# Performance work log

Measured on AMD Instinct MI355X. Metric: run time of the kernel, lower is better.

## Reference

```python
import jax, jax.numpy as jnp
import numpy as np
from jax import lax

VOCAB, EMBED, HIDDEN, LAYERS = 32000, 512, 1024, 2
B, S = 16, 256


def _lstm_layer(x_seq, h0, c0, W_ih, W_hh, b_ih, b_hh):
    # x_seq: [B, S, D]; PyTorch gate order: i, f, g, o
    def step(carry, x_t):
        h, c = carry
        gates = x_t @ W_ih.T + b_ih + h @ W_hh.T + b_hh  # [B, 4H]
        i, f, g, o = jnp.split(gates, 4, axis=-1)
        i = jax.nn.sigmoid(i); f = jax.nn.sigmoid(f)
        g = jnp.tanh(g); o = jax.nn.sigmoid(o)
        c = f * c + i * g
        h = o * jnp.tanh(c)
        return (h, c), h
    (hT, cT), hs = lax.scan(step, (h0, c0), jnp.swapaxes(x_seq, 0, 1))
    return jnp.swapaxes(hs, 0, 1), hT, cT  # [B,S,H], [B,H], [B,H]


def setup_inputs() -> dict:
    key = jax.random.key(0)
    ks = jax.random.split(key, 8)
    s_e = 1.0 / np.sqrt(EMBED)
    s_h = 1.0 / np.sqrt(HIDDEN)
    return {
        "x": jax.random.randint(ks[0], (B, S), 0, VOCAB),
        "h0": jnp.zeros((LAYERS, B, HIDDEN), jnp.float32),
        "c0": jnp.zeros((LAYERS, B, HIDDEN), jnp.float32),
        "emb": jax.random.normal(ks[1], (VOCAB, EMBED), jnp.float32),
        "W_ih0": jax.random.normal(ks[2], (4 * HIDDEN, EMBED), jnp.float32) * s_e,
        "W_hh0": jax.random.normal(ks[3], (4 * HIDDEN, HIDDEN), jnp.float32) * s_h,
        "b_ih0": jnp.zeros((4 * HIDDEN,), jnp.float32),
        "b_hh0": jnp.zeros((4 * HIDDEN,), jnp.float32),
        "W_ih1": jax.random.normal(ks[4], (4 * HIDDEN, HIDDEN), jnp.float32) * s_h,
        "W_hh1": jax.random.normal(ks[5], (4 * HIDDEN, HIDDEN), jnp.float32) * s_h,
        "b_ih1": jnp.zeros((4 * HIDDEN,), jnp.float32),
        "b_hh1": jnp.zeros((4 * HIDDEN,), jnp.float32),
        "fc_W": jax.random.normal(ks[6], (VOCAB, HIDDEN), jnp.float32) * s_h,
        "fc_b": jnp.zeros((VOCAB,), jnp.float32),
    }


def reference(x, h0, c0, emb, W_ih0, W_hh0, b_ih0, b_hh0,
              W_ih1, W_hh1, b_ih1, b_hh1, fc_W, fc_b):
    h = emb[x]  # [B, S, E] embedding lookup
    h, h1, c1 = _lstm_layer(h, h0[0], c0[0], W_ih0, W_hh0, b_ih0, b_hh0)
    h, h2, c2 = _lstm_layer(h, h0[1], c0[1], W_ih1, W_hh1, b_ih1, b_hh1)
    logits = h @ fc_W.T + fc_b  # [B, S, V]
    hT = jnp.stack([h1, h2])    # [L, B, H]
    cT = jnp.stack([c1, c2])
    return logits, hT, cT
```

## Files before the change

### kernel.cpp

```cpp
#include <hip/hip_runtime.h>
#include <hip/hip_bf16.h>
#include <cmath>

#define BATCH 16
#define SEQ 256
#define EMBED 512
#define HIDDEN 1024
#define GATES 4096
#define VOCAB 32000
#define MROWS 4096
#define LOGITS_SZ 131072000

#define NSLOT 257
#define SEQ_SLOTU16 16384
#define SEQ_LOU16 (NSLOT * SEQ_SLOTU16)

typedef unsigned int u32;
typedef unsigned short u16;
typedef unsigned long long u64;
typedef __attribute__((ext_vector_type(8))) short bf16x8;
typedef __attribute__((ext_vector_type(4))) float f32x4;

#define AS1 __attribute__((address_space(1)))
#define AS3 __attribute__((address_space(3)))

__device__ __forceinline__ u32 f2bf(float f) {
    u32 u = __float_as_uint(f);
    return (u + 0x7fffu + ((u >> 16) & 1u)) >> 16;
}
__device__ __forceinline__ float bf2f(u32 b) { return __uint_as_float(b << 16); }

__device__ __forceinline__ void astore(u64* p, u64 v) {
    __hip_atomic_store(p, v, __ATOMIC_RELAXED, __HIP_MEMORY_SCOPE_AGENT);
}

__global__ void embed_kernel(const int* __restrict__ x, const float* __restrict__ emb,
                             float* __restrict__ X0) {
    int r = blockIdx.x;
    int s = r >> 4, b = r & 15;
    int tok = x[b * SEQ + s];
    const float4* src = (const float4*)(emb + (size_t)tok * EMBED);
    float4* dst = (float4*)(X0 + (size_t)r * EMBED);
    for (int i = threadIdx.x; i < EMBED / 4; i += blockDim.x) dst[i] = src[i];
}

__global__ __launch_bounds__(256) void gemm_bt(
    const float* __restrict__ A, const float* __restrict__ B,
    const float* __restrict__ b1, const float* __restrict__ b2,
    float* __restrict__ C, int M, int N, int K, int perm) {
    __shared__ float As[8][128];
    __shared__ float Bs[8][128];
    int tid = threadIdx.x;
    int bm = blockIdx.y, bn = blockIdx.x;
    int arow = tid >> 1;
    int ak4 = (tid & 1) * 4;
    const float* Ag = A + (size_t)(bm * 128 + arow) * K + ak4;
    const float* Bg = B + (size_t)(bn * 128 + arow) * K + ak4;
    int tx = tid & 15, ty = tid >> 4;

    float acc[8][8];
#pragma unroll
    for (int i = 0; i < 8; i++)
#pragma unroll
        for (int j = 0; j < 8; j++) acc[i][j] = 0.f;

    for (int k0 = 0; k0 < K; k0 += 8) {
        float4 a4 = *(const float4*)(Ag + k0);
        float4 b4 = *(const float4*)(Bg + k0);
        __syncthreads();
        As[ak4 + 0][arow] = a4.x; As[ak4 + 1][arow] = a4.y;
        As[ak4 + 2][arow] = a4.z; As[ak4 + 3][arow] = a4.w;
        Bs[ak4 + 0][arow] = b4.x; Bs[ak4 + 1][arow] = b4.y;
        Bs[ak4 + 2][arow] = b4.z; Bs[ak4 + 3][arow] = b4.w;
        __syncthreads();
#pragma unroll
        for (int k = 0; k < 8; k++) {
            float av[8], bv[8];
            *(float4*)(av + 0) = *(const float4*)&As[k][ty * 8 + 0];
            *(float4*)(av + 4) = *(const float4*)&As[k][ty * 8 + 4];
            *(float4*)(bv + 0) = *(const float4*)&Bs[k][tx * 8 + 0];
            *(float4*)(bv + 4) = *(const float4*)&Bs[k][tx * 8 + 4];
#pragma unroll
            for (int i = 0; i < 8; i++)
#pragma unroll
                for (int j = 0; j < 8; j++) acc[i][j] += av[i] * bv[j];
        }
    }

#pragma unroll
    for (int i = 0; i < 8; i++) {
        int r = bm * 128 + ty * 8 + i;
        int orow = perm ? ((r & 15) * SEQ + (r >> 4)) : r;
#pragma unroll
        for (int j = 0; j < 8; j += 4) {
            int c = bn * 128 + tx * 8 + j;
            float4 v;
            float bb0 = (b1 ? b1[c + 0] : 0.f) + (b2 ? b2[c + 0] : 0.f);
            float bb1 = (b1 ? b1[c + 1] : 0.f) + (b2 ? b2[c + 1] : 0.f);
            float bb2 = (b1 ? b1[c + 2] : 0.f) + (b2 ? b2[c + 2] : 0.f);
            float bb3 = (b1 ? b1[c + 3] : 0.f) + (b2 ? b2[c + 3] : 0.f);
            v.x = acc[i][j + 0] + bb0;
            v.y = acc[i][j + 1] + bb1;
            v.z = acc[i][j + 2] + bb2;
            v.w = acc[i][j + 3] + bb3;
            *(float4*)&C[(size_t)orow * N + c] = v;
        }
    }
}

__global__ __launch_bounds__(256) void f32_to_bf16_kernel(
    const float* __restrict__ in, u16* __restrict__ out, int n8) {
    for (int i = blockIdx.x * 256 + threadIdx.x; i < n8; i += gridDim.x * 256) {
        float4 a = ((const float4*)in)[2 * (size_t)i + 0];
        float4 b = ((const float4*)in)[2 * (size_t)i + 1];
        uint4 o;
        o.x = f2bf(a.x) | (f2bf(a.y) << 16);
        o.y = f2bf(a.z) | (f2bf(a.w) << 16);
        o.z = f2bf(b.x) | (f2bf(b.y) << 16);
        o.w = f2bf(b.z) | (f2bf(b.w) << 16);
        ((uint4*)out)[i] = o;
    }
}

__global__ __launch_bounds__(256) void wih_swizzle_kernel(
    const float* __restrict__ W, u16* __restrict__ hi, u16* __restrict__ lo) {
    int bid = blockIdx.x, tid = threadIdx.x;
    int j0 = bid * 4;
#pragma unroll
    for (int i = 0; i < 8; i++) {
        int q = i * 256 + tid;
        int s32 = q >> 6, l = q & 63;
        int row = l & 15, hi4 = l >> 4;
        int nrow = (row >> 2) * HIDDEN + j0 + (row & 3);
        int k = s32 * 32 + hi4 * 8;
        const float* src = W + (size_t)nrow * HIDDEN + k;
        u32 hw[4], lw[4];
#pragma unroll
        for (int e = 0; e < 4; e++) {
            float x0 = src[2 * e], x1 = src[2 * e + 1];
            u32 h0 = f2bf(x0), h1 = f2bf(x1);
            hw[e] = h0 | (h1 << 16);
            lw[e] = f2bf(x0 - bf2f(h0)) | (f2bf(x1 - bf2f(h1)) << 16);
        }
        size_t e0 = (size_t)bid * 2048 + q;
        ((uint4*)hi)[e0] = make_uint4(hw[0], hw[1], hw[2], hw[3]);
        ((uint4*)lo)[e0] = make_uint4(lw[0], lw[1], lw[2], lw[3]);
    }
}

__global__ __launch_bounds__(256) void fc_mfma(
    const u16* __restrict__ Abf,
    const u16* __restrict__ Bbf,
    const float* __restrict__ bias,
    float* __restrict__ C) {
    const int K = HIDDEN;
    const int N = VOCAB;
    __shared__ char smem[16384];
    char* As = smem;
    char* Bs = smem + 8192;

    int tid = threadIdx.x;
    int w = tid >> 6, l = tid & 63;
    int bn = blockIdx.x, bm = blockIdx.y;
    int wr = w >> 1, wc = w & 1;
    int lr = l & 15, lk = l >> 4;

    f32x4 acc[4][4];
#pragma unroll
    for (int m = 0; m < 4; m++)
#pragma unroll
        for (int n = 0; n < 4; n++) acc[m][n] = {0.f, 0.f, 0.f, 0.f};

    int srow = tid >> 2, skc = (tid & 3) * 8;
    const u16* ga0 = Abf + (size_t)(bm * 128 + srow) * K + skc;
    const u16* ga1 = Abf + (size_t)(bm * 128 + 64 + srow) * K + skc;
    const u16* gb0 = Bbf + (size_t)(bn * 128 + srow) * K + skc;
    const u16* gb1 = Bbf + (size_t)(bn * 128 + 64 + srow) * K + skc;
    char* la0 = As + w * 1024;
    char* la1 = As + 4096 + w * 1024;
    char* lb0 = Bs + w * 1024;
    char* lb1 = Bs + 4096 + w * 1024;

    int afo[4], bfo[4];
#pragma unroll
    for (int m = 0; m < 4; m++) afo[m] = (wr * 64 + m * 16 + lr) * 64 + lk * 16;
#pragma unroll
    for (int n = 0; n < 4; n++) bfo[n] = (wc * 64 + n * 16 + lr) * 64 + lk * 16;

    for (int k0 = 0; k0 < K; k0 += 32) {
        __syncthreads();
        __builtin_amdgcn_global_load_lds((const AS1 u32*)(const void*)(ga0 + k0),
                                         (AS3 u32*)(void*)la0, 16, 0, 0);
        __builtin_amdgcn_global_load_lds((const AS1 u32*)(const void*)(ga1 + k0),
                                         (AS3 u32*)(void*)la1, 16, 0, 0);
        __builtin_amdgcn_global_load_lds((const AS1 u32*)(const void*)(gb0 + k0),
                                         (AS3 u32*)(void*)lb0, 16, 0, 0);
        __builtin_amdgcn_global_load_lds((const AS1 u32*)(const void*)(gb1 + k0),
                                         (AS3 u32*)(void*)lb1, 16, 0, 0);
        __syncthreads();

        bf16x8 af[4], bfr[4];
#pragma unroll
        for (int m = 0; m < 4; m++) af[m] = *(const bf16x8*)(As + afo[m]);
#pragma unroll
        for (int n = 0; n < 4; n++) bfr[n] = *(const bf16x8*)(Bs + bfo[n]);
#pragma unroll
        for (int m = 0; m < 4; m++)
#pragma unroll
            for (int n = 0; n < 4; n++)
                acc[m][n] = __builtin_amdgcn_mfma_f32_16x16x32_bf16(
                    af[m], bfr[n], acc[m][n], 0, 0, 0);
    }

    int rbase = bm * 128 + wr * 64 + lk * 4;
    int cbase = bn * 128 + wc * 64 + lr;
#pragma unroll
    for (int m = 0; m < 4; m++) {
#pragma unroll
        for (int n = 0; n < 4; n++) {
            int c = cbase + n * 16;
            float bb = bias[c];
#pragma unroll
            for (int j = 0; j < 4; j++) {
                int r = rbase + m * 16 + j;
                int orow = (r & 15) * SEQ + (r >> 4);
                C[(size_t)orow * N + c] = acc[m][n][j] + bb;
            }
        }
    }
}

__global__ __launch_bounds__(256, 1) void lstm_fused(
    const float* __restrict__ Whh0, const float* __restrict__ Whh1,
    const float* __restrict__ G0,
    const u16* __restrict__ wih_hi,
    const u16* __restrict__ wih_lo,
    const float* __restrict__ bi1, const float* __restrict__ bh1,
    const float* __restrict__ c0in,
    float* __restrict__ c_tail, float* __restrict__ h_tail,
    u16* __restrict__ seq0, u16* __restrict__ seq1,
    u32* __restrict__ arrive) {
    __shared__ __align__(16) char lds[139264];
    char* W0hi = lds;
    char* W0lo = lds + 32768;
    char* W1hi = lds + 65536;
    char* W1lo = lds + 98304;
    float* Pw = (float*)(lds + 131072);

    const int tid = threadIdx.x;
    const int bid = blockIdx.x;
    const int j0 = bid * 4;
    const int w = tid >> 6, l = tid & 63;
    const int lb = l & 15, hi4 = l >> 4, xr = l & 7;

#pragma unroll
    for (int lay = 0; lay < 2; lay++) {
        const float* Whh = lay ? Whh1 : Whh0;
        char* dH = lay ? W1hi : W0hi;
        char* dL = lay ? W1lo : W0lo;
        for (int i = 0; i < 8; i++) {
            int q = i * 256 + tid;
            int row = q >> 7, cin = q & 127;
            int nrow = (row >> 2) * HIDDEN + j0 + (row & 3);
            const float* src = Whh + (size_t)nrow * HIDDEN + cin * 8;
            int dst = row * 2048 + ((cin ^ (row & 7)) << 4);
            u32 hw[4], lw[4];
#pragma unroll
            for (int e = 0; e < 4; e++) {
                float x0 = src[2 * e], x1 = src[2 * e + 1];
                u32 hb0 = f2bf(x0), hb1 = f2bf(x1);
                hw[e] = hb0 | (hb1 << 16);
                lw[e] = f2bf(x0 - bf2f(hb0)) | (f2bf(x1 - bf2f(hb1)) << 16);
            }
            *(uint4*)(dH + dst) = make_uint4(hw[0], hw[1], hw[2], hw[3]);
            *(uint4*)(dL + dst) = make_uint4(lw[0], lw[1], lw[2], lw[3]);
        }
    }

    float c0r = 0.f, c1r = 0.f;
    float g00 = 0, g01 = 0, g02 = 0, g03 = 0;
    float g10 = 0, g11 = 0, g12 = 0, g13 = 0;
    if (tid < 64) {
        c0r = c0in[lb * HIDDEN + j0 + hi4];
        c1r = c0in[16384 + lb * HIDDEN + j0 + hi4];
        const float* gp = G0 + (size_t)lb * GATES + j0 + hi4;
        g00 = gp[0]; g01 = gp[HIDDEN]; g02 = gp[2 * HIDDEN]; g03 = gp[3 * HIDDEN];
        g10 = bi1[j0 + hi4] + bh1[j0 + hi4];
        g11 = bi1[HIDDEN + j0 + hi4] + bh1[HIDDEN + j0 + hi4];
        g12 = bi1[2 * HIDDEN + j0 + hi4] + bh1[2 * HIDDEN + j0 + hi4];
        g13 = bi1[3 * HIDDEN + j0 + hi4] + bh1[3 * HIDDEN + j0 + hi4];
    }
    __syncthreads();

    const u64* s0h = (const u64*)seq0;
    const u64* s0l = (const u64*)(seq0 + SEQ_LOU16);
    const u64* s1h = (const u64*)seq1;
    const u64* s1l = (const u64*)(seq1 + SEQ_LOU16);
    const int fb = lb * 256 + hi4 * 2;
    const size_t wbase = (size_t)bid * 2048 + l;

    union u4bf { uint4 u; bf16x8 v; };

    for (int s = 0; s <= SEQ; s++) {
        const bool actL0 = (s < SEQ);
        const bool actL1 = (s >= 1);

        u4bf xh8[8], xl8[8], yh8[8], yl8[8];
        {
            const int base = s * 4096 + fb;
#pragma unroll
            for (int ss = 0; ss < 8; ss++) {
                const int idx = base + (w * 8 + ss) * 8;
                xh8[ss].u = *(const uint4*)(s0h + idx);
                xl8[ss].u = *(const uint4*)(s0l + idx);
            }
        }
        if (actL1) {
            const int base = (s - 1) * 4096 + fb;
#pragma unroll
            for (int ss = 0; ss < 8; ss++) {
                const int idx = base + (w * 8 + ss) * 8;
                yh8[ss].u = *(const uint4*)(s1h + idx);
                yl8[ss].u = *(const uint4*)(s1l + idx);
            }
        }

        if (actL0) {
            f32x4 a0 = {0.f,0.f,0.f,0.f}, a1 = {0.f,0.f,0.f,0.f}, a2 = {0.f,0.f,0.f,0.f};
#pragma unroll
            for (int ss = 0; ss < 8; ss++) {
                const int s32 = w * 8 + ss;
                const int off = lb * 2048 + (((s32 * 4 + hi4) ^ xr) << 4);
                bf16x8 ah = *(const bf16x8*)(W0hi + off);
                bf16x8 al = *(const bf16x8*)(W0lo + off);
                a0 = __builtin_amdgcn_mfma_f32_16x16x32_bf16(ah, xh8[ss].v, a0, 0, 0, 0);
                a1 = __builtin_amdgcn_mfma_f32_16x16x32_bf16(al, xh8[ss].v, a1, 0, 0, 0);
                a2 = __builtin_amdgcn_mfma_f32_16x16x32_bf16(ah, xl8[ss].v, a2, 0, 0, 0);
            }
            f32x4 v0 = a0 + a1 + a2;
            *(f32x4*)&Pw[((0 * 4 + w) * 64 + l) * 4] = v0;
        }

        if (actL1) {
            f32x4 a0 = {0.f,0.f,0.f,0.f}, a1 = {0.f,0.f,0.f,0.f}, a2 = {0.f,0.f,0.f,0.f};
#pragma unroll
            for (int ss = 0; ss < 8; ss++) {
                const size_t e = wbase + (size_t)(w * 8 + ss) * 64;
                bf16x8 ah = *(const bf16x8*)(wih_hi + e * 8);
                bf16x8 al = *(const bf16x8*)(wih_lo + e * 8);
                a0 = __builtin_amdgcn_mfma_f32_16x16x32_bf16(ah, xh8[ss].v, a0, 0, 0, 0);
                a1 = __builtin_amdgcn_mfma_f32_16x16x32_bf16(al, xh8[ss].v, a1, 0, 0, 0);
                a2 = __builtin_amdgcn_mfma_f32_16x16x32_bf16(ah, xl8[ss].v, a2, 0, 0, 0);
            }
#pragma unroll
            for (int ss = 0; ss < 8; ss++) {
                const int s32 = w * 8 + ss;
                const int off = lb * 2048 + (((s32 * 4 + hi4) ^ xr) << 4);
                bf16x8 ah = *(const bf16x8*)(W1hi + off);
                bf16x8 al = *(const bf16x8*)(W1lo + off);
                a0 = __builtin_amdgcn_mfma_f32_16x16x32_bf16(ah, yh8[ss].v, a0, 0, 0, 0);
                a1 = __builtin_amdgcn_mfma_f32_16x16x32_bf16(al, yh8[ss].v, a1, 0, 0, 0);
                a2 = __builtin_amdgcn_mfma_f32_16x16x32_bf16(ah, yl8[ss].v, a2, 0, 0, 0);
            }
            f32x4 v1 = a0 + a1 + a2;
            *(f32x4*)&Pw[((1 * 4 + w) * 64 + l) * 4] = v1;
        }
        __syncthreads();

        if (tid < 64) {
            if (actL0) {
                float pre[4];
#pragma unroll
                for (int g = 0; g < 4; g++) {
                    const int ll = (g << 4) | lb;
                    pre[g] = Pw[((0 * 4 + 0) * 64 + ll) * 4 + hi4]
                           + Pw[((0 * 4 + 1) * 64 + ll) * 4 + hi4]
                           + Pw[((0 * 4 + 2) * 64 + ll) * 4 + hi4]
                           + Pw[((0 * 4 + 3) * 64 + ll) * 4 + hi4];
                }
                const float ig = 1.f / (1.f + __expf(-(pre[0] + g00)));
                const float fg = 1.f / (1.f + __expf(-(pre[1] + g01)));
                const float gt = tanhf(pre[2] + g02);
                const float og = 1.f / (1.f + __expf(-(pre[3] + g03)));
                c0r = fg * c0r + ig * gt;
                const float hv = og * tanhf(c0r);
                if (s == SEQ - 1) {
                    h_tail[lb * HIDDEN + j0 + hi4] = hv;
                    c_tail[lb * HIDDEN + j0 + hi4] = c0r;
                }
                float q0 = __shfl(hv, 0 + l), q1 = __shfl(hv, 16 + l);
                float q2 = __shfl(hv, 32 + l), q3 = __shfl(hv, 48 + l);
                if (l < 16) {
                    u32 hb0 = f2bf(q0), hb1 = f2bf(q1), hb2 = f2bf(q2), hb3 = f2bf(q3);
                    u64 hq = (u64)(hb0 | (hb1 << 16)) | ((u64)(hb2 | (hb3 << 16)) << 32);
                    u32 lb0 = f2bf(q0 - bf2f(hb0)), lb1 = f2bf(q1 - bf2f(hb1));
                    u32 lb2 = f2bf(q2 - bf2f(hb2)), lb3 = f2bf(q3 - bf2f(hb3));
                    u64 lq = (u64)(lb0 | (lb1 << 16)) | ((u64)(lb2 | (lb3 << 16)) << 32);
                    const int iq = (s + 1) * 4096 + l * 256 + bid;
                    astore((u64*)seq0 + iq, hq);
                    astore((u64*)(seq0 + SEQ_LOU16) + iq, lq);
                }
            }
            if (actL1) {
                float pre[4];
#pragma unroll
                for (int g = 0; g < 4; g++) {
                    const int ll = (g << 4) | lb;
                    pre[g] = Pw[((1 * 4 + 0) * 64 + ll) * 4 + hi4]
                           + Pw[((1 * 4 + 1) * 64 + ll) * 4 + hi4]
                           + Pw[((1 * 4 + 2) * 64 + ll) * 4 + hi4]
                           + Pw[((1 * 4 + 3) * 64 + ll) * 4 + hi4];
                }
                const float ig = 1.f / (1.f + __expf(-(pre[0] + g10)));
                const float fg = 1.f / (1.f + __expf(-(pre[1] + g11)));
                const float gt = tanhf(pre[2] + g12);
                const float og = 1.f / (1.f + __expf(-(pre[3] + g13)));
                c1r = fg * c1r + ig * gt;
                const float hv = og * tanhf(c1r);
                if (s == SEQ) {
                    h_tail[16384 + lb * HIDDEN + j0 + hi4] = hv;
                    c_tail[16384 + lb * HIDDEN + j0 + hi4] = c1r;
                }
                float q0 = __shfl(hv, 0 + l), q1 = __shfl(hv, 16 + l);
                float q2 = __shfl(hv, 32 + l), q3 = __shfl(hv, 48 + l);
                if (l < 16) {
                    u32 hb0 = f2bf(q0), hb1 = f2bf(q1), hb2 = f2bf(q2), hb3 = f2bf(q3);
                    u64 hq = (u64)(hb0 | (hb1 << 16)) | ((u64)(hb2 | (hb3 << 16)) << 32);
                    u32 lb0 = f2bf(q0 - bf2f(hb0)), lb1 = f2bf(q1 - bf2f(hb1));
                    u32 lb2 = f2bf(q2 - bf2f(hb2)), lb3 = f2bf(q3 - bf2f(hb3));
                    u64 lq = (u64)(lb0 | (lb1 << 16)) | ((u64)(lb2 | (lb3 << 16)) << 32);
                    const int iq = s * 4096 + l * 256 + bid;
                    astore((u64*)seq1 + iq, hq);
                    astore((u64*)(seq1 + SEQ_LOU16) + iq, lq);
                }
            }
        }

        if (s < SEQ) {
            if (tid < 64) {
                asm volatile("s_waitcnt vmcnt(0)" ::: "memory");
                if (tid == 0)
                    __hip_atomic_store(&arrive[bid], (u32)(s + 1), __ATOMIC_RELAXED,
                                       __HIP_MEMORY_SCOPE_AGENT);
                if (s + 1 < SEQ) {
                    const float* gp = G0 + (size_t)((s + 1) * BATCH + lb) * GATES + j0 + hi4;
                    g00 = gp[0]; g01 = gp[HIDDEN];
                    g02 = gp[2 * HIDDEN]; g03 = gp[3 * HIDDEN];
                }
                const u32 epoch = (u32)(s + 1);
                const int i0 = l * 4;
                for (;;) {
                    u32 q0 = __hip_atomic_load(&arrive[i0 + 0], __ATOMIC_RELAXED,
                                               __HIP_MEMORY_SCOPE_AGENT);
                    u32 q1 = __hip_atomic_load(&arrive[i0 + 1], __ATOMIC_RELAXED,
                                               __HIP_MEMORY_SCOPE_AGENT);
                    u32 q2 = __hip_atomic_load(&arrive[i0 + 2], __ATOMIC_RELAXED,
                                               __HIP_MEMORY_SCOPE_AGENT);
                    u32 q3 = __hip_atomic_load(&arrive[i0 + 3], __ATOMIC_RELAXED,
                                               __HIP_MEMORY_SCOPE_AGENT);
                    u32 m01 = q0 < q1 ? q0 : q1;
                    u32 m23 = q2 < q3 ? q2 : q3;
                    u32 mn = m01 < m23 ? m01 : m23;
                    if (__all(mn >= epoch)) break;
                    __builtin_amdgcn_s_sleep(2);
                }
                asm volatile("" ::: "memory");
            }
            __syncthreads();
        }
    }
}

__global__ void init_state(const float* __restrict__ h0, u16* __restrict__ seq0,
                           u16* __restrict__ seq1, u32* __restrict__ arrive) {
    int gid = blockIdx.x * 256 + threadIdx.x;
    if (gid < 256) arrive[gid] = 0;
    int layer = gid >> 14, b = (gid >> 10) & 15, j = gid & 1023;
    float h = h0[gid];
    u32 hb = f2bf(h);
    u32 lbits = f2bf(h - bf2f(hb));
    u16* sq = layer ? seq1 : seq0;
    sq[b * 1024 + j] = (u16)hb;
    sq[SEQ_LOU16 + b * 1024 + j] = (u16)lbits;
}

__global__ void write_tails(const float* __restrict__ h_tail, const float* __restrict__ c_tail,
                            float* __restrict__ out) {
    int gid = blockIdx.x * 256 + threadIdx.x;
    out[LOGITS_SZ + gid] = h_tail[gid];
    out[LOGITS_SZ + 32768 + gid] = c_tail[gid];
}

extern "C" void kernel_launch(void* const* d_in, const int* in_sizes, int n_in,
                              void* d_out, int out_size, void* d_ws, size_t ws_size,
                              hipStream_t stream) {
    const int* x = (const int*)d_in[0];
    const float* h0 = (const float*)d_in[1];
    const float* c0 = (const float*)d_in[2];
    const float* emb = (const float*)d_in[3];
    const float* W_ih0 = (const float*)d_in[4];
    const float* W_hh0 = (const float*)d_in[5];
    const float* b_ih0 = (const float*)d_in[6];
    const float* b_hh0 = (const float*)d_in[7];
    const float* W_ih1 = (const float*)d_in[8];
    const float* W_hh1 = (const float*)d_in[9];
    const float* b_ih1 = (const float*)d_in[10];
    const float* b_hh1 = (const float*)d_in[11];
    const float* fc_W = (const float*)d_in[12];
    const float* fc_b = (const float*)d_in[13];
    float* out = (float*)d_out;
    float* ws = (float*)d_ws;

    const size_t OFF_G = 0;
    const size_t OFF_X0 = OFF_G + (size_t)MROWS * GATES;
    const size_t OFF_SEQ0 = OFF_X0 + (size_t)MROWS * EMBED;
    const size_t SEQ_FLOATS = (size_t)2 * NSLOT * SEQ_SLOTU16 / 2;
    const size_t OFF_SEQ1 = OFF_SEQ0 + SEQ_FLOATS;
    const size_t OFF_WIHH = OFF_SEQ1 + SEQ_FLOATS;
    const size_t OFF_WIHL = OFF_WIHH + (size_t)GATES * HIDDEN / 2;
    const size_t OFF_HT = OFF_WIHL + (size_t)GATES * HIDDEN / 2;
    const size_t OFF_CT = OFF_HT + 2 * BATCH * HIDDEN;
    const size_t OFF_AR = OFF_CT + 2 * BATCH * HIDDEN;

    u16* seq0 = (u16*)(ws + OFF_SEQ0);
    u16* seq1 = (u16*)(ws + OFF_SEQ1);
    u16* wihH = (u16*)(ws + OFF_WIHH);
    u16* wihL = (u16*)(ws + OFF_WIHL);
    u32* arrive = (u32*)(ws + OFF_AR);

    init_state<<<128, 256, 0, stream>>>(h0, seq0, seq1, arrive);
    embed_kernel<<<MROWS, 128, 0, stream>>>(x, emb, ws + OFF_X0);
    wih_swizzle_kernel<<<256, 256, 0, stream>>>(W_ih1, wihH, wihL);

    gemm_bt<<<dim3(GATES / 128, MROWS / 128), 256, 0, stream>>>(
        ws + OFF_X0, W_ih0, b_ih0, b_hh0, ws + OFF_G, MROWS, GATES, EMBED, 0);

    {
        const float* Whh0p = W_hh0;
        const float* Whh1p = W_hh1;
        const float* Gp = ws + OFF_G;
        const u16* wh = wihH;
        const u16* wl = wihL;
        const float* bi = b_ih1;
        const float* bh = b_hh1;
        const float* ci = c0;
        float* ct = ws + OFF_CT;
        float* ht = ws + OFF_HT;
        u16* s0 = seq0;
        u16* s1 = seq1;
        u32* ar = arrive;
        void* args[] = {(void*)&Whh0p, (void*)&Whh1p, (void*)&Gp, (void*)&wh,
                        (void*)&wl, (void*)&bi, (void*)&bh, (void*)&ci,
                        (void*)&ct, (void*)&ht, (void*)&s0, (void*)&s1, (void*)&ar};
        hipLaunchCooperativeKernel((void*)lstm_fused, dim3(256), dim3(256), args, 0, stream);
    }

    f32_to_bf16_kernel<<<4096, 256, 0, stream>>>(fc_W, (u16*)(ws + OFF_G), VOCAB * HIDDEN / 8);
    fc_mfma<<<dim3(VOCAB / 128, MROWS / 128), 256, 0, stream>>>(
        seq1 + SEQ_SLOTU16, (const u16*)(ws + OFF_G), fc_b, out);

    write_tails<<<128, 256, 0, stream>>>(ws + OFF_HT, ws + OFF_CT, out);
}
```

Before: 4.015 ms.

## Replace FP32 layer-0 input projection GEMM with split-bf16 MFMA kernel

The fp32 SIMT GEMM for the layer-0 input projection (4096x4096x512) is replaced with an MFMA kernel using a three-term hi/lo bf16 split to approximate fp32 accuracy. The embedding gather now writes hi/lo bf16 halves directly, and W_ih0 is converted to hi/lo each call. The goal is to move this GEMM onto matrix cores. In exchange it adds a weight conversion pass and triples the MFMA count, and it drops the lo*lo term, which slightly changes precision.

```diff
diff --git a/kernel.cpp b/kernel.cpp
--- a/kernel.cpp
+++ b/kernel.cpp
@@ -34,78 +34,21 @@
     __hip_atomic_store(p, v, __ATOMIC_RELAXED, __HIP_MEMORY_SCOPE_AGENT);
 }
 
-__global__ void embed_kernel(const int* __restrict__ x, const float* __restrict__ emb,
-                             float* __restrict__ X0) {
+__global__ void embed_hl_kernel(const int* __restrict__ x, const float* __restrict__ emb,
+                                u16* __restrict__ XH, u16* __restrict__ XL) {
     int r = blockIdx.x;
     int s = r >> 4, b = r & 15;
     int tok = x[b * SEQ + s];
     const float4* src = (const float4*)(emb + (size_t)tok * EMBED);
-    float4* dst = (float4*)(X0 + (size_t)r * EMBED);
-    for (int i = threadIdx.x; i < EMBED / 4; i += blockDim.x) dst[i] = src[i];
-}
-
-__global__ __launch_bounds__(256) void gemm_bt(
-    const float* __restrict__ A, const float* __restrict__ B,
-    const float* __restrict__ b1, const float* __restrict__ b2,
-    float* __restrict__ C, int M, int N, int K, int perm) {
-    __shared__ float As[8][128];
-    __shared__ float Bs[8][128];
-    int tid = threadIdx.x;
-    int bm = blockIdx.y, bn = blockIdx.x;
-    int arow = tid >> 1;
-    int ak4 = (tid & 1) * 4;
-    const float* Ag = A + (size_t)(bm * 128 + arow) * K + ak4;
-    const float* Bg = B + (size_t)(bn * 128 + arow) * K + ak4;
-    int tx = tid & 15, ty = tid >> 4;
-
-    float acc[8][8];
-#pragma unroll
-    for (int i = 0; i < 8; i++)
-#pragma unroll
-        for (int j = 0; j < 8; j++) acc[i][j] = 0.f;
-
-    for (int k0 = 0; k0 < K; k0 += 8) {
-        float4 a4 = *(const float4*)(Ag + k0);
-        float4 b4 = *(const float4*)(Bg + k0);
-        __syncthreads();
-        As[ak4 + 0][arow] = a4.x; As[ak4 + 1][arow] = a4.y;
-        As[ak4 + 2][arow] = a4.z; As[ak4 + 3][arow] = a4.w;
-        Bs[ak4 + 0][arow] = b4.x; Bs[ak4 + 1][arow] = b4.y;
-        Bs[ak4 + 2][arow] = b4.z; Bs[ak4 + 3][arow] = b4.w;
-        __syncthreads();
-#pragma unroll
-        for (int k = 0; k < 8; k++) {
-            float av[8], bv[8];
-            *(float4*)(av + 0) = *(const float4*)&As[k][ty * 8 + 0];
-            *(float4*)(av + 4) = *(const float4*)&As[k][ty * 8 + 4];
-            *(float4*)(bv + 0) = *(const float4*)&Bs[k][tx * 8 + 0];
-            *(float4*)(bv + 4) = *(const float4*)&Bs[k][tx * 8 + 4];
-#pragma unroll
-            for (int i = 0; i < 8; i++)
-#pragma unroll
-                for (int j = 0; j < 8; j++) acc[i][j] += av[i] * bv[j];
-        }
-    }
-
-#pragma unroll
-    for (int i = 0; i < 8; i++) {
-        int r = bm * 128 + ty * 8 + i;
-        int orow = perm ? ((r & 15) * SEQ + (r >> 4)) : r;
-#pragma unroll
-        for (int j = 0; j < 8; j += 4) {
-            int c = bn * 128 + tx * 8 + j;
-            float4 v;
-            float bb0 = (b1 ? b1[c + 0] : 0.f) + (b2 ? b2[c + 0] : 0.f);
-            float bb1 = (b1 ? b1[c + 1] : 0.f) + (b2 ? b2[c + 1] : 0.f);
-            float bb2 = (b1 ? b1[c + 2] : 0.f) + (b2 ? b2[c + 2] : 0.f);
-            float bb3 = (b1 ? b1[c + 3] : 0.f) + (b2 ? b2[c + 3] : 0.f);
-            v.x = acc[i][j + 0] + bb0;
-            v.y = acc[i][j + 1] + bb1;
-            v.z = acc[i][j + 2] + bb2;
-            v.w = acc[i][j + 3] + bb3;
-            *(float4*)&C[(size_t)orow * N + c] = v;
-        }
-    }
+    int i = threadIdx.x;
+    float4 a = src[i];
+    u32 h0 = f2bf(a.x), h1 = f2bf(a.y), h2 = f2bf(a.z), h3 = f2bf(a.w);
+    u64 hq = (u64)(h0 | (h1 << 16)) | ((u64)(h2 | (h3 << 16)) << 32);
+    u32 l0 = f2bf(a.x - bf2f(h0)), l1 = f2bf(a.y - bf2f(h1));
+    u32 l2 = f2bf(a.z - bf2f(h2)), l3 = f2bf(a.w - bf2f(h3));
+    u64 lq = (u64)(l0 | (l1 << 16)) | ((u64)(l2 | (l3 << 16)) << 32);
+    ((u64*)(XH + (size_t)r * EMBED))[i] = hq;
+    ((u64*)(XL + (size_t)r * EMBED))[i] = lq;
 }
 
 __global__ __launch_bounds__(256) void f32_to_bf16_kernel(
@@ -122,6 +65,20 @@
     }
 }
 
+__global__ __launch_bounds__(256) void f32_to_bf16hl_kernel(
+    const float* __restrict__ in, u16* __restrict__ hi, u16* __restrict__ lo, int n4) {
+    for (int i = blockIdx.x * 256 + threadIdx.x; i < n4; i += gridDim.x * 256) {
+        float4 a = ((const float4*)in)[i];
+        u32 h0 = f2bf(a.x), h1 = f2bf(a.y), h2 = f2bf(a.z), h3 = f2bf(a.w);
+        u64 hq = (u64)(h0 | (h1 << 16)) | ((u64)(h2 | (h3 << 16)) << 32);
+        u32 l0 = f2bf(a.x - bf2f(h0)), l1 = f2bf(a.y - bf2f(h1));
+        u32 l2 = f2bf(a.z - bf2f(h2)), l3 = f2bf(a.w - bf2f(h3));
+        u64 lq = (u64)(l0 | (l1 << 16)) | ((u64)(l2 | (l3 << 16)) << 32);
+        ((u64*)hi)[i] = hq;
+        ((u64*)lo)[i] = lq;
+    }
+}
+
 __global__ __launch_bounds__(256) void wih_swizzle_kernel(
     const float* __restrict__ W, u16* __restrict__ hi, u16* __restrict__ lo) {
     int bid = blockIdx.x, tid = threadIdx.x;
@@ -145,6 +102,109 @@
         size_t e0 = (size_t)bid * 2048 + q;
         ((uint4*)hi)[e0] = make_uint4(hw[0], hw[1], hw[2], hw[3]);
         ((uint4*)lo)[e0] = make_uint4(lw[0], lw[1], lw[2], lw[3]);
+    }
+}
+
+__global__ __launch_bounds__(256) void xproj_mfma(
+    const u16* __restrict__ Ahi, const u16* __restrict__ Alo,
+    const u16* __restrict__ Bhi, const u16* __restrict__ Blo,
+    const float* __restrict__ b1, const float* __restrict__ b2,
+    float* __restrict__ C) {
+    const int K = EMBED;
+    const int N = GATES;
+    __shared__ char smem[32768];
+    char* AsH = smem;
+    char* AsL = smem + 8192;
+    char* BsH = smem + 16384;
+    char* BsL = smem + 24576;
+
+    int tid = threadIdx.x;
+    int w = tid >> 6, l = tid & 63;
+    int bn = blockIdx.x, bm = blockIdx.y;
+    int wr = w >> 1, wc = w & 1;
+    int lr = l & 15, lk = l >> 4;
+
+    f32x4 acc[4][4];
+#pragma unroll
+    for (int m = 0; m < 4; m++)
+#pragma unroll
+        for (int n = 0; n < 4; n++) acc[m][n] = {0.f, 0.f, 0.f, 0.f};
+
+    int srow = tid >> 2, skc = (tid & 3) * 8;
+    const u16* gah0 = Ahi + (size_t)(bm * 128 + srow) * K + skc;
+    const u16* gah1 = Ahi + (size_t)(bm * 128 + 64 + srow) * K + skc;
+    const u16* gal0 = Alo + (size_t)(bm * 128 + srow) * K + skc;
+    const u16* gal1 = Alo + (size_t)(bm * 128 + 64 + srow) * K + skc;
+    const u16* gbh0 = Bhi + (size_t)(bn * 128 + srow) * K + skc;
+    const u16* gbh1 = Bhi + (size_t)(bn * 128 + 64 + srow) * K + skc;
+    const u16* gbl0 = Blo + (size_t)(bn * 128 + srow) * K + skc;
+    const u16* gbl1 = Blo + (size_t)(bn * 128 + 64 + srow) * K + skc;
+    char* lah0 = AsH + w * 1024;       char* lah1 = AsH + 4096 + w * 1024;
+    char* lal0 = AsL + w * 1024;       char* lal1 = AsL + 4096 + w * 1024;
+    char* lbh0 = BsH + w * 1024;       char* lbh1 = BsH + 4096 + w * 1024;
+    char* lbl0 = BsL + w * 1024;       char* lbl1 = BsL + 4096 + w * 1024;
+
+    int afo[4], bfo[4];
+#pragma unroll
+    for (int m = 0; m < 4; m++) afo[m] = (wr * 64 + m * 16 + lr) * 64 + lk * 16;
+#pragma unroll
+    for (int n = 0; n < 4; n++) bfo[n] = (wc * 64 + n * 16 + lr) * 64 + lk * 16;
+
+    for (int k0 = 0; k0 < K; k0 += 32) {
+        __syncthreads();
+        __builtin_amdgcn_global_load_lds((const AS1 u32*)(const void*)(gah0 + k0),
+                                         (AS3 u32*)(void*)lah0, 16, 0, 0);
+        __builtin_amdgcn_global_load_lds((const AS1 u32*)(const void*)(gah1 + k0),
+                                         (AS3 u32*)(void*)lah1, 16, 0, 0);
+        __builtin_amdgcn_global_load_lds((const AS1 u32*)(const void*)(gal0 + k0),
+                                         (AS3 u32*)(void*)lal0, 16, 0, 0);
+        __builtin_amdgcn_global_load_lds((const AS1 u32*)(const void*)(gal1 + k0),
+                                         (AS3 u32*)(void*)lal1, 16, 0, 0);
+        __builtin_amdgcn_global_load_lds((const AS1 u32*)(const void*)(gbh0 + k0),
+                                         (AS3 u32*)(void*)lbh0, 16, 0, 0);
+        __builtin_amdgcn_global_load_lds((const AS1 u32*)(const void*)(gbh1 + k0),
+                                         (AS3 u32*)(void*)lbh1, 16, 0, 0);
+        __builtin_amdgcn_global_load_lds((const AS1 u32*)(const void*)(gbl0 + k0),
+                                         (AS3 u32*)(void*)lbl0, 16, 0, 0);
+        __builtin_amdgcn_global_load_lds((const AS1 u32*)(const void*)(gbl1 + k0),
+                                         (AS3 u32*)(void*)lbl1, 16, 0, 0);
+        __syncthreads();
+
+        bf16x8 ah[4], al[4], bh[4], bl[4];
+#pragma unroll
+        for (int m = 0; m < 4; m++) {
+            ah[m] = *(const bf16x8*)(AsH + afo[m]);
+            al[m] = *(const bf16x8*)(AsL + afo[m]);
+        }
+#pragma unroll
+        for (int n = 0; n < 4; n++) {
+            bh[n] = *(const bf16x8*)(BsH + bfo[n]);
+            bl[n] = *(const bf16x8*)(BsL + bfo[n]);
+        }
+#pragma unroll
+        for (int m = 0; m < 4; m++)
+#pragma unroll
+            for (int n = 0; n < 4; n++) {
+                acc[m][n] = __builtin_amdgcn_mfma_f32_16x16x32_bf16(ah[m], bh[n], acc[m][n], 0, 0, 0);
+                acc[m][n] = __builtin_amdgcn_mfma_f32_16x16x32_bf16(al[m], bh[n], acc[m][n], 0, 0, 0);
+                acc[m][n] = __builtin_amdgcn_mfma_f32_16x16x32_bf16(ah[m], bl[n], acc[m][n], 0, 0, 0);
+            }
+    }
+
+    int rbase = bm * 128 + wr * 64 + lk * 4;
+    int cbase = bn * 128 + wc * 64 + lr;
+#pragma unroll
+    for (int m = 0; m < 4; m++) {
+#pragma unroll
+        for (int n = 0; n < 4; n++) {
+            int c = cbase + n * 16;
+            float bb = b1[c] + b2[c];
+#pragma unroll
+            for (int j = 0; j < 4; j++) {
+                int r = rbase + m * 16 + j;
+                C[(size_t)r * N + c] = acc[m][n][j] + bb;
+            }
+        }
     }
 }
 
@@ -512,28 +572,36 @@
     float* ws = (float*)d_ws;
 
     const size_t OFF_G = 0;
-    const size_t OFF_X0 = OFF_G + (size_t)MROWS * GATES;
-    const size_t OFF_SEQ0 = OFF_X0 + (size_t)MROWS * EMBED;
+    const size_t OFF_X0H = OFF_G + (size_t)MROWS * GATES;
+    const size_t OFF_X0L = OFF_X0H + (size_t)MROWS * EMBED / 2;
+    const size_t OFF_SEQ0 = OFF_X0L + (size_t)MROWS * EMBED / 2;
     const size_t SEQ_FLOATS = (size_t)2 * NSLOT * SEQ_SLOTU16 / 2;
     const size_t OFF_SEQ1 = OFF_SEQ0 + SEQ_FLOATS;
     const size_t OFF_WIHH = OFF_SEQ1 + SEQ_FLOATS;
     const size_t OFF_WIHL = OFF_WIHH + (size_t)GATES * HIDDEN / 2;
-    const size_t OFF_HT = OFF_WIHL + (size_t)GATES * HIDDEN / 2;
+    const size_t OFF_W0H = OFF_WIHL + (size_t)GATES * HIDDEN / 2;
+    const size_t OFF_W0L = OFF_W0H + (size_t)GATES * EMBED / 2;
+    const size_t OFF_HT = OFF_W0L + (size_t)GATES * EMBED / 2;
     const size_t OFF_CT = OFF_HT + 2 * BATCH * HIDDEN;
     const size_t OFF_AR = OFF_CT + 2 * BATCH * HIDDEN;
 
+    u16* x0H = (u16*)(ws + OFF_X0H);
+    u16* x0L = (u16*)(ws + OFF_X0L);
     u16* seq0 = (u16*)(ws + OFF_SEQ0);
     u16* seq1 = (u16*)(ws + OFF_SEQ1);
     u16* wihH = (u16*)(ws + OFF_WIHH);
     u16* wihL = (u16*)(ws + OFF_WIHL);
+    u16* w0H = (u16*)(ws + OFF_W0H);
+    u16* w0L = (u16*)(ws + OFF_W0L);
     u32* arrive = (u32*)(ws + OFF_AR);
 
     init_state<<<128, 256, 0, stream>>>(h0, seq0, seq1, arrive);
-    embed_kernel<<<MROWS, 128, 0, stream>>>(x, emb, ws + OFF_X0);
+    embed_hl_kernel<<<MROWS, 128, 0, stream>>>(x, emb, x0H, x0L);
     wih_swizzle_kernel<<<256, 256, 0, stream>>>(W_ih1, wihH, wihL);
-
-    gemm_bt<<<dim3(GATES / 128, MROWS / 128), 256, 0, stream>>>(
-        ws + OFF_X0, W_ih0, b_ih0, b_hh0, ws + OFF_G, MROWS, GATES, EMBED, 0);
+    f32_to_bf16hl_kernel<<<2048, 256, 0, stream>>>(W_ih0, w0H, w0L, GATES * EMBED / 4);
+
+    xproj_mfma<<<dim3(GATES / 128, MROWS / 128), 256, 0, stream>>>(
+        x0H, x0L, w0H, w0L, b_ih0, b_hh0, ws + OFF_G);
 
     {
         const float* Whh0p = W_hh0;
```

New measurement: 3.865 ms. 1.04x faster.
